# Optimization experiments

Measured on AMD Instinct MI355X. Metric: run time of the kernel, lower is better.

The kernel has to match this reference:

```python
import jax, jax.numpy as jnp
import numpy as np

B, T, W, N, D, H, E, NB = 1, 2048, 15, 512, 1024, 150, 20, 10
CP = 2  # coref_prop iterations
NEG = 1e23


def _bucket(d):
    # Lee-et-al style distance bucketing into NB=10 buckets
    d = jnp.clip(d, 0, None)
    logd = (jnp.floor(jnp.log(jnp.maximum(d.astype(jnp.float32), 1.0)) / np.log(2.0)).astype(jnp.int32) + 3)
    return jnp.clip(jnp.where(d <= 4, d, logd), 0, NB - 1)


def _pairs(u, begin, end, Wl, bl, Wr, br, Wp, bp, Edist, Wd, bd, W1, b1, Wo, bo):
    # OptFFpairs: left + right + prod*prod + dist-embedding -> 2-layer FF -> scalar
    l = u @ Wl + bl                                   # [B,N,H]
    r = u @ Wr + br
    s = u @ Wp + bp
    dist = _bucket(begin[:, :, None] - end[:, None, :])  # [B,N,N]
    pe = Edist[dist] @ Wd + bd                        # [B,N,N,H]
    h = l[:, :, None, :] + r[:, None, :, :] + s[:, :, None, :] * s[:, None, :, :] + pe
    h = jax.nn.relu(h)
    h = jax.nn.relu(h @ W1 + b1)
    return (h @ Wo + bo)[..., 0]                      # [B,N,N]


def _add_scores(cs, ss):
    # coref_add_scores: add unary span scores symmetrically, zero the diagonal
    s = cs + ss + jnp.swapaxes(ss, -1, -2)            # ss: [B,N,1]
    eye = jnp.eye(s.shape[-1], dtype=s.dtype)
    return s * (1.0 - eye)


def _overwrite_spans(all_vecs, idx, lengths, values):
    b, t, w, d = all_vecs.shape
    flat = all_vecs.reshape(b, t * w, d)
    k = idx.shape[1]
    mask = (jnp.arange(k)[None, :] < lengths[:, None])[..., None]   # [B,K,1]
    bidx = jnp.arange(b)[:, None]
    orig = flat[bidx, idx]                                          # [B,K,D]
    flat = flat.at[bidx, idx].set(jnp.where(mask, values, orig))
    return flat.reshape(b, t, w, d)


def setup_inputs() -> dict:
    key = jax.random.key(0)
    ks = jax.random.split(key, 24)
    sc = 0.02
    inp = {
        'all_span_vecs': jax.random.normal(ks[0], (B, T, W, D), jnp.float32),
        'span_vecs': jax.random.normal(ks[1], (B, N, D), jnp.float32),
        'span_scores': jax.random.normal(ks[2], (B, N, 1), jnp.float32),
        'triangular_mask': jnp.tril(jnp.ones((N, N), jnp.float32))[None].repeat(B, 0),
        'span_begin': jnp.sort(jax.random.randint(ks[3], (B, N), 0, T), axis=-1).astype(jnp.int32),
        'span_end': jax.random.randint(ks[4], (B, N), 0, T).astype(jnp.int32),
        'prune_indices': jnp.sort(jax.random.permutation(ks[5], T * W)[:N])[None].astype(jnp.int64),
        'span_lengths': jnp.full((B,), N, jnp.int32),
        # OptFFpairs params
        'Wl': jax.random.normal(ks[6], (D, H)) * sc, 'bl': jnp.zeros((H,)),
        'Wr': jax.random.normal(ks[7], (D, H)) * sc, 'br': jnp.zeros((H,)),
        'Wp': jax.random.normal(ks[8], (D, H)) * sc, 'bp': jnp.zeros((H,)),
        'Edist': jax.random.normal(ks[9], (NB, E)) * sc,
        'Wd': jax.random.normal(ks[10], (E, H)) * sc, 'bd': jnp.zeros((H,)),
        'W1': jax.random.normal(ks[11], (H, H)) * sc, 'b1': jnp.zeros((H,)),
        'Wo': jax.random.normal(ks[12], (H, 1)) * sc, 'bo': jnp.zeros((1,)),
        # MyGate params
        'Wg': jax.random.normal(ks[13], (2 * D, D)) * sc, 'bg': jnp.zeros((D,)),
        # coref_pruner params
        'Wpr': jax.random.normal(ks[14], (D, 1)) * sc, 'bpr': jnp.zeros((1,)),
    }
    return inp


def reference(all_span_vecs, span_vecs, span_scores, triangular_mask,
              Wl, bl, Wr, br, Wp, bp, Edist, Wd, bd, W1, b1, Wo, bo,
              Wg, bg, Wpr, bpr,
              span_begin, span_end, prune_indices, span_lengths):
    pargs = (Wl, bl, Wr, br, Wp, bp, Edist, Wd, bd, W1, b1, Wo, bo)
    update = span_vecs
    scores = _pairs(update, span_begin, span_end, *pargs)
    scores = _add_scores(scores, span_scores)
    for _ in range(CP):
        probs = jax.nn.softmax(scores - (1.0 - triangular_mask) * NEG, axis=-1)
        ctxt = jnp.einsum('bij,bjd->bid', probs, update)
        g = jax.nn.sigmoid(jnp.concatenate([update, ctxt], axis=-1) @ Wg + bg)
        update = g * update + (1.0 - g) * ctxt
        scores = _pairs(update, span_begin, span_end, *pargs)
        scores = _add_scores(scores, update @ Wpr + bpr)
    all_out = _overwrite_spans(all_span_vecs, prune_indices, span_lengths, update)
    return (all_out, update, scores)
```

## Files before the change

### kernel.cpp

```cpp
#include <hip/hip_runtime.h>
#include <hip/hip_bf16.h>
#include <cstdint>
#include <cstddef>

typedef __attribute__((ext_vector_type(8))) short short8;
typedef __attribute__((ext_vector_type(4))) float floatx4;

#define MFMA_BF16(a,b,c) __builtin_amdgcn_mfma_f32_16x16x32_bf16((a),(b),(c),0,0,0)

__device__ __forceinline__ float bf2f(short s) {
    return __uint_as_float(((unsigned int)(unsigned short)s) << 16);
}
__device__ __forceinline__ unsigned short f2bf(float f) {
    unsigned int u = __float_as_uint(f);
    u += 0x7FFFu + ((u >> 16) & 1u);
    return (unsigned short)(u >> 16);
}
__device__ __forceinline__ int bucketd(int d) {
    if (d < 0) d = 0;
    if (d <= 4) return d;
    int b = 34 - __clz(d);
    return b > 9 ? 9 : b;
}

__global__ __launch_bounds__(256) void k_prep(
    const float* __restrict__ Wg, const float* __restrict__ Wl, const float* __restrict__ Wr,
    const float* __restrict__ Wp, const float* __restrict__ Wpr,
    const float* __restrict__ span_vecs, const float* __restrict__ span_scores,
    const float* __restrict__ W1g, const float* __restrict__ Edist,
    const float* __restrict__ Wd, const float* __restrict__ bd,
    const float* __restrict__ b1, const float* __restrict__ Wo,
    const float* __restrict__ bl, const float* __restrict__ br, const float* __restrict__ bp,
    const float* __restrict__ bpr,
    unsigned short* __restrict__ WgT, unsigned short* __restrict__ WprojT,
    unsigned short* __restrict__ updT, unsigned short* __restrict__ ubf0,
    float* __restrict__ updatef, float* __restrict__ ss0,
    unsigned short* __restrict__ W1T, unsigned short* __restrict__ Pb,
    float* __restrict__ b1p, float* __restrict__ wop, float* __restrict__ bproj)
{
    __shared__ float tile[32][33];
    int b = blockIdx.x, tid = threadIdx.x;
    if (b < 3040) {
        const float* in; unsigned short* out; int R, C, ldo, rb, cb;
        if (b < 2048)      { in = Wg; out = WgT; R = 2048; C = 1024; ldo = 2048; rb = (b & 63) * 32; cb = (b >> 6) * 32; }
        else if (b < 2208) { int t = b - 2048; in = Wl; out = WprojT;            R = 1024; C = 150; ldo = 1024; rb = (t & 31) * 32; cb = (t >> 5) * 32; }
        else if (b < 2368) { int t = b - 2208; in = Wr; out = WprojT + 192*1024; R = 1024; C = 150; ldo = 1024; rb = (t & 31) * 32; cb = (t >> 5) * 32; }
        else if (b < 2528) { int t = b - 2368; in = Wp; out = WprojT + 384*1024; R = 1024; C = 150; ldo = 1024; rb = (t & 31) * 32; cb = (t >> 5) * 32; }
        else               { int t = b - 2528; in = span_vecs; out = updT;       R = 512;  C = 1024; ldo = 512;  rb = (t & 15) * 32; cb = (t >> 4) * 32; }
        int tx = tid & 31, ty = tid >> 5;
#pragma unroll
        for (int k = 0; k < 4; ++k) {
            int r = rb + ty + k*8, c = cb + tx;
            if (r < R && c < C) tile[ty + k*8][tx] = in[(size_t)r*C + c];
        }
        __syncthreads();
#pragma unroll
        for (int k = 0; k < 4; ++k) {
            int c = cb + ty + k*8, r = rb + tx;
            if (r < R && c < C) out[(size_t)c*ldo + r] = f2bf(tile[tx][ty + k*8]);
        }
        return;
    }
    int g = (b - 3040) * 256 + tid;
    const int gsz = 512 * 256;
    for (int i = g; i < 512*1024; i += gsz) {
        float v = span_vecs[i];
        updatef[i] = v;
        ubf0[(i >> 10)*2048 + (i & 1023)] = f2bf(v);
    }
    for (int i = g; i < 512; i += gsz) ss0[i] = span_scores[i];
    for (int i = g; i < 160*168; i += gsz) {
        int n = i / 168, k = i % 168;
        W1T[i] = f2bf((n < 150 && k < 150) ? W1g[k*150 + n] : 0.f);
    }
    for (int i = g; i < 10*168; i += gsz) {
        int bk = i / 168, h = i % 168;
        float v = 0.f;
        if (h < 150) {
            v = bd[h];
            for (int e = 0; e < 20; ++e) v += Edist[bk*20 + e] * Wd[e*150 + h];
        }
        Pb[i] = f2bf(v);
    }
    for (int i = g; i < 160; i += gsz) {
        b1p[i] = (i < 150) ? b1[i] : 0.f;
        wop[i] = (i < 150) ? Wo[i] : 0.f;
    }
    for (int i = g; i < 640; i += gsz) {
        float v = 0.f;
        if (i < 150) v = bl[i];
        else if (i >= 192 && i < 342) v = br[i - 192];
        else if (i >= 384 && i < 534) v = bp[i - 384];
        else if (i == 576) v = bpr[0];
        bproj[i] = v;
    }
    for (int i = g; i < 42*1024; i += gsz) { WprojT[150*1024 + i] = 0; WprojT[342*1024 + i] = 0; WprojT[534*1024 + i] = 0; }
    for (int i = g; i < 1024; i += gsz) WprojT[576*1024 + i] = f2bf(Wpr[i]);
    for (int i = g; i < 63*1024; i += gsz) WprojT[577*1024 + i] = 0;
}

__global__ __launch_bounds__(256) void k_gemm64(
    const unsigned short* __restrict__ A, int lda,
    const unsigned short* __restrict__ BT, int ldb,
    int K, const float* __restrict__ bias,
    float* __restrict__ Cf, int ldc,
    unsigned short* __restrict__ Cb, int ldcb,
    const float* __restrict__ uf, const float* __restrict__ cf,
    float* __restrict__ uout, unsigned short* __restrict__ updTout,
    float* __restrict__ ss1, int mode)
{
    __shared__ __align__(16) unsigned short As[64*72];
    __shared__ __align__(16) unsigned short Bs[64*72];
    int tid = threadIdx.x;
    int lane = tid & 63, w = tid >> 6;
    int wy = w >> 1, wx = w & 1;
    int ln15 = lane & 15, kg = lane >> 4;
    int m0 = blockIdx.x * 64, n0 = blockIdx.y * 64;
    int r0 = tid >> 3, c8 = (tid & 7) * 8;
    const unsigned short* pA0 = A + (size_t)(m0 + r0)*lda + c8;
    const unsigned short* pA1 = pA0 + (size_t)32*lda;
    const unsigned short* pB0 = BT + (size_t)(n0 + r0)*ldb + c8;
    const unsigned short* pB1 = pB0 + (size_t)32*ldb;
    floatx4 acc[2][2] = {};
    uint4 va0 = *(const uint4*)pA0, va1 = *(const uint4*)pA1;
    uint4 vb0 = *(const uint4*)pB0, vb1 = *(const uint4*)pB1;
    for (int kb = 0; kb < K; kb += 64) {
        __syncthreads();
        *(uint4*)(&As[r0*72 + c8])        = va0;
        *(uint4*)(&As[(r0 + 32)*72 + c8]) = va1;
        *(uint4*)(&Bs[r0*72 + c8])        = vb0;
        *(uint4*)(&Bs[(r0 + 32)*72 + c8]) = vb1;
        __syncthreads();
        int kn = kb + 64;
        if (kn < K) {
            va0 = *(const uint4*)(pA0 + kn); va1 = *(const uint4*)(pA1 + kn);
            vb0 = *(const uint4*)(pB0 + kn); vb1 = *(const uint4*)(pB1 + kn);
        }
#pragma unroll
        for (int ks = 0; ks < 2; ++ks) {
            int ko = ks*32 + kg*8;
            short8 a0 = *(const short8*)(&As[(wy*32 + ln15)*72 + ko]);
            short8 a1 = *(const short8*)(&As[(wy*32 + 16 + ln15)*72 + ko]);
            short8 b0 = *(const short8*)(&Bs[(wx*32 + ln15)*72 + ko]);
            short8 b1 = *(const short8*)(&Bs[(wx*32 + 16 + ln15)*72 + ko]);
            acc[0][0] = MFMA_BF16(a0, b0, acc[0][0]);
            acc[0][1] = MFMA_BF16(a0, b1, acc[0][1]);
            acc[1][0] = MFMA_BF16(a1, b0, acc[1][0]);
            acc[1][1] = MFMA_BF16(a1, b1, acc[1][1]);
        }
    }
#pragma unroll
    for (int mt = 0; mt < 2; ++mt)
#pragma unroll
    for (int nt = 0; nt < 2; ++nt) {
        int n  = n0 + wx*32 + nt*16 + ln15;
        int mb = m0 + wy*32 + mt*16 + kg*4;
        if (mode == 0) {
            float b_ = bias[n];
#pragma unroll
            for (int rg = 0; rg < 4; ++rg) {
                float v = acc[mt][nt][rg] + b_;
                Cb[(size_t)(mb + rg)*ldcb + n] = f2bf(v);
                if (n == 576) ss1[mb + rg] = v;
            }
        } else if (mode == 1) {
#pragma unroll
            for (int rg = 0; rg < 4; ++rg) {
                float v = acc[mt][nt][rg];
                Cf[(size_t)(mb + rg)*ldc + n] = v;
                Cb[(size_t)(mb + rg)*ldcb + n] = f2bf(v);
            }
        } else {
            float b_ = bias[n];
            ushort4 tv;
            unsigned short* tvp = &tv.x;
#pragma unroll
            for (int rg = 0; rg < 4; ++rg) {
                float v = acc[mt][nt][rg] + b_;
                float gg = 1.f / (1.f + __expf(-v));
                size_t off = (size_t)(mb + rg)*1024 + n;
                float nu = gg*uf[off] + (1.f - gg)*cf[off];
                uout[off] = nu;
                unsigned short nb = f2bf(nu);
                Cb[(size_t)(mb + rg)*ldcb + n] = nb;
                tvp[rg] = nb;
            }
            *(ushort4*)(updTout + (size_t)n*512 + mb) = tv;
        }
    }
}

__global__ __launch_bounds__(256) void k_softmax(const float* __restrict__ scores,
                                                 unsigned short* __restrict__ probsb)
{
    int i = blockIdx.x;
    int tid = threadIdx.x;
    int lane = tid & 63, w = tid >> 6;
    __shared__ float red[8];
    int j0 = tid, j1 = tid + 256;
    bool v0 = (j0 <= i), v1 = (j1 <= i);
    float x0 = v0 ? scores[(size_t)i*512 + j0] : -1e30f;
    float x1 = v1 ? scores[(size_t)i*512 + j1] : -1e30f;
    float mx = fmaxf(x0, x1);
    for (int off = 32; off; off >>= 1) mx = fmaxf(mx, __shfl_xor(mx, off));
    if (lane == 0) red[w] = mx;
    __syncthreads();
    mx = fmaxf(fmaxf(red[0], red[1]), fmaxf(red[2], red[3]));
    float p0 = v0 ? __expf(x0 - mx) : 0.f;
    float p1 = v1 ? __expf(x1 - mx) : 0.f;
    float sm = p0 + p1;
    for (int off = 32; off; off >>= 1) sm += __shfl_xor(sm, off);
    if (lane == 0) red[4 + w] = sm;
    __syncthreads();
    float inv = 1.f / (red[4] + red[5] + red[6] + red[7]);
    probsb[(size_t)i*512 + j0] = f2bf(p0 * inv);
    probsb[(size_t)i*512 + j1] = f2bf(p1 * inv);
}

__global__ __launch_bounds__(512, 2) void k_pair(
    const unsigned short* __restrict__ lrsb,
    const unsigned short* __restrict__ Pb,
    const unsigned short* __restrict__ W1Tg,
    const float* __restrict__ b1p, const float* __restrict__ wop,
    const float* __restrict__ bo,
    const float* __restrict__ ssbuf,
    const int* __restrict__ beginp, const int* __restrict__ endp,
    float* __restrict__ scoresOut)
{
    __shared__ __align__(16) unsigned short smR[74*168];
    int tid = threadIdx.x;
    int i0 = blockIdx.x * 16, j0 = blockIdx.y * 16;
    for (int c = tid; c < 74*21; c += 512) {
        int row = c / 21, c8 = (c % 21) * 8;
        const unsigned short* src;
        if (row < 16)      src = lrsb + (size_t)(i0 + row)*640 + c8;
        else if (row < 32) src = lrsb + (size_t)(i0 + row - 16)*640 + 384 + c8;
        else if (row < 48) src = lrsb + (size_t)(j0 + row - 32)*640 + 192 + c8;
        else if (row < 64) src = lrsb + (size_t)(j0 + row - 48)*640 + 384 + c8;
        else               src = Pb + (size_t)(row - 64)*168 + c8;
        *(uint4*)(&smR[row*168 + c8]) = *(const uint4*)src;
    }
    int lane = tid & 63, w = tid >> 6;
    int ln15 = lane & 15, kg = lane >> 4;
    int iw = i0 + 2*w;
    int ej = endp[j0 + ln15];
    int da = bucketd(beginp[iw] - ej);
    int db = bucketd(beginp[iw + 1] - ej);
    __syncthreads();
    floatx4 acc[2][10] = {};
    for (int kb = 0; kb < 5; ++kb) {
        int ko = kb*32 + kg*8;
        short8 bv[10];
#pragma unroll
        for (int nt = 0; nt < 10; ++nt)
            bv[nt] = *(const short8*)(W1Tg + (size_t)(nt*16 + ln15)*168 + ko);
        short8 rv  = *(const short8*)(&smR[(32 + ln15)*168 + ko]);
        short8 sjv = *(const short8*)(&smR[(48 + ln15)*168 + ko]);
        short8 hf[2];
#pragma unroll
        for (int mt = 0; mt < 2; ++mt) {
            int ri = 2*w + mt;
            short8 lv  = *(const short8*)(&smR[ri*168 + ko]);
            short8 siv = *(const short8*)(&smR[(16 + ri)*168 + ko]);
            int d = mt ? db : da;
            short8 pv  = *(const short8*)(&smR[(64 + d)*168 + ko]);
#pragma unroll
            for (int t = 0; t < 8; ++t) {
                float h = bf2f(lv[t]) + bf2f(rv[t]) + bf2f(siv[t]) * bf2f(sjv[t]) + bf2f(pv[t]);
                h = fmaxf(h, 0.f);
                hf[mt][t] = (short)f2bf(h);
            }
        }
#pragma unroll
        for (int nt = 0; nt < 10; ++nt) {
            acc[0][nt] = MFMA_BF16(hf[0], bv[nt], acc[0][nt]);
            acc[1][nt] = MFMA_BF16(hf[1], bv[nt], acc[1][nt]);
        }
    }
    float part[2][4] = {};
#pragma unroll
    for (int nt = 0; nt < 10; ++nt) {
        int n = nt*16 + ln15;
        float b1v = b1p[n], wv = wop[n];
#pragma unroll
        for (int mt = 0; mt < 2; ++mt)
#pragma unroll
            for (int rg = 0; rg < 4; ++rg)
                part[mt][rg] += fmaxf(acc[mt][nt][rg] + b1v, 0.f) * wv;
    }
    float bo0 = bo[0];
#pragma unroll
    for (int mt = 0; mt < 2; ++mt) {
#pragma unroll
        for (int rg = 0; rg < 4; ++rg) {
            float p = part[mt][rg];
            p += __shfl_xor(p, 1); p += __shfl_xor(p, 2);
            p += __shfl_xor(p, 4); p += __shfl_xor(p, 8);
            part[mt][rg] = p;
        }
        if (ln15 == 0) {
            int i = iw + mt;
            float ssi = ssbuf[i];
            int jb = j0 + kg*4;
            float r0 = part[mt][0] + bo0 + ssi + ssbuf[jb + 0]; if (i == jb + 0) r0 = 0.f;
            float r1 = part[mt][1] + bo0 + ssi + ssbuf[jb + 1]; if (i == jb + 1) r1 = 0.f;
            float r2 = part[mt][2] + bo0 + ssi + ssbuf[jb + 2]; if (i == jb + 2) r2 = 0.f;
            float r3 = part[mt][3] + bo0 + ssi + ssbuf[jb + 3]; if (i == jb + 3) r3 = 0.f;
            float4 vv; vv.x = r0; vv.y = r1; vv.z = r2; vv.w = r3;
            *(float4*)(scoresOut + (size_t)i*512 + jb) = vv;
        }
    }
}

__global__ __launch_bounds__(256) void k_final(const float* __restrict__ allv,
                                               const int* __restrict__ prune,
                                               const int* __restrict__ lengths,
                                               const float* __restrict__ updatef,
                                               float* __restrict__ out)
{
    int row = blockIdx.x;
    if (row < 30720) {
        int len = lengths[0];
        if (len > 512) len = 512;
        int lo = 0, hi = len;
        while (lo < hi) { int mid = (lo + hi) >> 1; if (prune[mid] < row) lo = mid + 1; else hi = mid; }
        bool found = (lo < len) && (prune[lo] == row);
        const float4* src = found ? (const float4*)(updatef + (size_t)lo*1024)
                                  : (const float4*)(allv + (size_t)row*1024);
        ((float4*)(out + (size_t)row*1024))[threadIdx.x] = src[threadIdx.x];
    } else {
        int k = row - 30720;
        ((float4*)(out + (size_t)row*1024))[threadIdx.x] =
            ((const float4*)(updatef + (size_t)k*1024))[threadIdx.x];
    }
}

extern "C" void kernel_launch(void* const* d_in, const int* in_sizes, int n_in,
                              void* d_out, int out_size, void* d_ws, size_t ws_size,
                              hipStream_t stream) {
    const float* all_span    = (const float*)d_in[0];
    const float* span_vecs   = (const float*)d_in[1];
    const float* span_scores = (const float*)d_in[2];
    const int*   beginp      = (const int*)d_in[4];
    const int*   endp        = (const int*)d_in[5];
    const int*   prune       = (const int*)d_in[6];
    const int*   lengths     = (const int*)d_in[7];
    const float* Wl = (const float*)d_in[8];  const float* bl = (const float*)d_in[9];
    const float* Wr = (const float*)d_in[10]; const float* br = (const float*)d_in[11];
    const float* Wp = (const float*)d_in[12]; const float* bp = (const float*)d_in[13];
    const float* Edist = (const float*)d_in[14];
    const float* Wd = (const float*)d_in[15]; const float* bd = (const float*)d_in[16];
    const float* W1 = (const float*)d_in[17]; const float* b1 = (const float*)d_in[18];
    const float* Wo = (const float*)d_in[19]; const float* bo = (const float*)d_in[20];
    const float* Wg = (const float*)d_in[21]; const float* bg = (const float*)d_in[22];
    const float* Wpr = (const float*)d_in[23]; const float* bpr = (const float*)d_in[24];

    char* wsb = (char*)d_ws;
    size_t o = 0;
    auto nxt = [&](size_t b) { size_t r = o; o += (b + 255) & ~(size_t)255; return r; };
    float* updatef  = (float*)(wsb + nxt(512*1024*4));
    float* ctxtf    = (float*)(wsb + nxt(512*1024*4));
    float* scoresws = (float*)(wsb + nxt(512*512*4));
    float* ss0      = (float*)(wsb + nxt(512*4));
    float* ss1      = (float*)(wsb + nxt(512*4));
    float* bproj    = (float*)(wsb + nxt(640*4));
    float* b1p      = (float*)(wsb + nxt(160*4));
    float* wop      = (float*)(wsb + nxt(160*4));
    unsigned short* ubf0    = (unsigned short*)(wsb + nxt(512*2048*2));
    unsigned short* ubf1    = (unsigned short*)(wsb + nxt(512*2048*2));
    unsigned short* updT    = (unsigned short*)(wsb + nxt(1024*512*2));
    unsigned short* probsb  = (unsigned short*)(wsb + nxt(512*512*2));
    unsigned short* lrsb    = (unsigned short*)(wsb + nxt(512*640*2));
    unsigned short* WgT     = (unsigned short*)(wsb + nxt(1024*2048*2));
    unsigned short* WprojT  = (unsigned short*)(wsb + nxt(640*1024*2));
    unsigned short* W1T     = (unsigned short*)(wsb + nxt(160*168*2));
    unsigned short* Pb      = (unsigned short*)(wsb + nxt(10*168*2));

    float* outp = (float*)d_out;
    float* out_scores = outp + 31457280 + 524288;

    k_prep<<<3552, 256, 0, stream>>>(Wg, Wl, Wr, Wp, Wpr, span_vecs, span_scores,
                                     W1, Edist, Wd, bd, b1, Wo, bl, br, bp, bpr,
                                     WgT, WprojT, updT, ubf0, updatef, ss0,
                                     W1T, Pb, b1p, wop, bproj);

    k_gemm64<<<dim3(8, 10), 256, 0, stream>>>(ubf0, 2048, WprojT, 1024, 1024, bproj,
                                              nullptr, 0, lrsb, 640,
                                              nullptr, nullptr, nullptr, nullptr, ss1, 0);
    k_pair<<<dim3(32, 32), 512, 0, stream>>>(lrsb, Pb, W1T, b1p, wop, bo, ss0, beginp, endp, scoresws);

    unsigned short* ucur = ubf0;
    unsigned short* unxt = ubf1;
    for (int it = 0; it < 2; ++it) {
        k_softmax<<<512, 256, 0, stream>>>(scoresws, probsb);
        k_gemm64<<<dim3(8, 16), 256, 0, stream>>>(probsb, 512, updT, 512, 512, nullptr,
                                                  ctxtf, 1024, ucur + 1024, 2048,
                                                  nullptr, nullptr, nullptr, nullptr, nullptr, 1);
        k_gemm64<<<dim3(8, 16), 256, 0, stream>>>(ucur, 2048, WgT, 2048, 2048, bg,
                                                  nullptr, 0, unxt, 2048,
                                                  updatef, ctxtf, updatef, updT, nullptr, 2);
        k_gemm64<<<dim3(8, 10), 256, 0, stream>>>(unxt, 2048, WprojT, 1024, 1024, bproj,
                                                  nullptr, 0, lrsb, 640,
                                                  nullptr, nullptr, nullptr, nullptr, ss1, 0);
        float* sdst = (it == 1) ? out_scores : scoresws;
        k_pair<<<dim3(32, 32), 512, 0, stream>>>(lrsb, Pb, W1T, b1p, wop, bo, ss1, beginp, endp, sdst);
        unsigned short* t = ucur; ucur = unxt; unxt = t;
    }

    k_final<<<31232, 256, 0, stream>>>(all_span, prune, lengths, updatef, outp);
}
```

Baseline: 514.9 us.

## Shrink GEMM M-tile to 32 with deeper prefetch; stage W1 in LDS for pair kernel

The GEMM kernel drops from 64x64 to 32x64 tiles, which doubles the grid (128 to 256 blocks for the larger GEMMs) to better fill the many CUs. It also prefetches global data two K-steps ahead through a pair of register buffers and adds an occupancy hint. The pair kernel now stages each 32-wide K slice of W1 into double-buffered shared memory with register prefetch, instead of having every wave read the W1 fragments straight from global memory. This adds LDS use and a barrier per K step in the pair kernel, and smaller GEMM tiles mean less reuse of each loaded B tile.

Result: slower. 536.6 us (+4.2%).

```diff
diff --git a/kernel.cpp b/kernel.cpp
--- a/kernel.cpp
+++ b/kernel.cpp
@@ -99,84 +99,81 @@
     for (int i = g; i < 63*1024; i += gsz) WprojT[577*1024 + i] = 0;
 }
 
-__global__ __launch_bounds__(256) void k_gemm64(
+__global__ __launch_bounds__(256, 4) void k_gemm(
     const unsigned short* __restrict__ A, int lda,
     const unsigned short* __restrict__ BT, int ldb,
     int K, const float* __restrict__ bias,
-    float* __restrict__ Cf, int ldc,
+    float* __restrict__ Cf,
     unsigned short* __restrict__ Cb, int ldcb,
     const float* __restrict__ uf, const float* __restrict__ cf,
     float* __restrict__ uout, unsigned short* __restrict__ updTout,
     float* __restrict__ ss1, int mode)
 {
-    __shared__ __align__(16) unsigned short As[64*72];
+    __shared__ __align__(16) unsigned short As[32*72];
     __shared__ __align__(16) unsigned short Bs[64*72];
     int tid = threadIdx.x;
     int lane = tid & 63, w = tid >> 6;
     int wy = w >> 1, wx = w & 1;
     int ln15 = lane & 15, kg = lane >> 4;
-    int m0 = blockIdx.x * 64, n0 = blockIdx.y * 64;
-    int r0 = tid >> 3, c8 = (tid & 7) * 8;
-    const unsigned short* pA0 = A + (size_t)(m0 + r0)*lda + c8;
-    const unsigned short* pA1 = pA0 + (size_t)32*lda;
-    const unsigned short* pB0 = BT + (size_t)(n0 + r0)*ldb + c8;
+    int m0 = blockIdx.x * 32, n0 = blockIdx.y * 64;
+    int rA = tid >> 3, c8 = (tid & 7) * 8;
+    const unsigned short* pA  = A  + (size_t)(m0 + rA)*lda + c8;
+    const unsigned short* pB0 = BT + (size_t)(n0 + rA)*ldb + c8;
     const unsigned short* pB1 = pB0 + (size_t)32*ldb;
-    floatx4 acc[2][2] = {};
-    uint4 va0 = *(const uint4*)pA0, va1 = *(const uint4*)pA1;
-    uint4 vb0 = *(const uint4*)pB0, vb1 = *(const uint4*)pB1;
-    for (int kb = 0; kb < K; kb += 64) {
+    int nk = K >> 6;
+    uint4 ra[2], rb0[2], rb1[2];
+    ra[0]  = *(const uint4*)pA;        ra[1]  = *(const uint4*)(pA + 64);
+    rb0[0] = *(const uint4*)pB0;       rb0[1] = *(const uint4*)(pB0 + 64);
+    rb1[0] = *(const uint4*)pB1;       rb1[1] = *(const uint4*)(pB1 + 64);
+    floatx4 acc[2] = {};
+    for (int k = 0; k < nk; ++k) {
+        int cur = k & 1;
         __syncthreads();
-        *(uint4*)(&As[r0*72 + c8])        = va0;
-        *(uint4*)(&As[(r0 + 32)*72 + c8]) = va1;
-        *(uint4*)(&Bs[r0*72 + c8])        = vb0;
-        *(uint4*)(&Bs[(r0 + 32)*72 + c8]) = vb1;
+        *(uint4*)(&As[rA*72 + c8])        = ra[cur];
+        *(uint4*)(&Bs[rA*72 + c8])        = rb0[cur];
+        *(uint4*)(&Bs[(rA + 32)*72 + c8]) = rb1[cur];
+        int kn = (k + 2) << 6;
+        if (kn < K) {
+            ra[cur]  = *(const uint4*)(pA + kn);
+            rb0[cur] = *(const uint4*)(pB0 + kn);
+            rb1[cur] = *(const uint4*)(pB1 + kn);
+        }
         __syncthreads();
-        int kn = kb + 64;
-        if (kn < K) {
-            va0 = *(const uint4*)(pA0 + kn); va1 = *(const uint4*)(pA1 + kn);
-            vb0 = *(const uint4*)(pB0 + kn); vb1 = *(const uint4*)(pB1 + kn);
-        }
 #pragma unroll
         for (int ks = 0; ks < 2; ++ks) {
             int ko = ks*32 + kg*8;
-            short8 a0 = *(const short8*)(&As[(wy*32 + ln15)*72 + ko]);
-            short8 a1 = *(const short8*)(&As[(wy*32 + 16 + ln15)*72 + ko]);
+            short8 a  = *(const short8*)(&As[(wy*16 + ln15)*72 + ko]);
             short8 b0 = *(const short8*)(&Bs[(wx*32 + ln15)*72 + ko]);
             short8 b1 = *(const short8*)(&Bs[(wx*32 + 16 + ln15)*72 + ko]);
-            acc[0][0] = MFMA_BF16(a0, b0, acc[0][0]);
-            acc[0][1] = MFMA_BF16(a0, b1, acc[0][1]);
-            acc[1][0] = MFMA_BF16(a1, b0, acc[1][0]);
-            acc[1][1] = MFMA_BF16(a1, b1, acc[1][1]);
-        }
-    }
-#pragma unroll
-    for (int mt = 0; mt < 2; ++mt)
+            acc[0] = MFMA_BF16(a, b0, acc[0]);
+            acc[1] = MFMA_BF16(a, b1, acc[1]);
+        }
+    }
 #pragma unroll
     for (int nt = 0; nt < 2; ++nt) {
         int n  = n0 + wx*32 + nt*16 + ln15;
-        int mb = m0 + wy*32 + mt*16 + kg*4;
+        int mb = m0 + wy*16 + kg*4;
         if (mode == 0) {
             float b_ = bias[n];
 #pragma unroll
             for (int rg = 0; rg < 4; ++rg) {
-                float v = acc[mt][nt][rg] + b_;
+                float v = acc[nt][rg] + b_;
                 Cb[(size_t)(mb + rg)*ldcb + n] = f2bf(v);
                 if (n == 576) ss1[mb + rg] = v;
             }
         } else if (mode == 1) {
 #pragma unroll
             for (int rg = 0; rg < 4; ++rg) {
-                float v = acc[mt][nt][rg];
-                Cf[(size_t)(mb + rg)*ldc + n] = v;
+                float v = acc[nt][rg];
+                Cf[(size_t)(mb + rg)*1024 + n] = v;
                 Cb[(size_t)(mb + rg)*ldcb + n] = f2bf(v);
             }
         } else {
             float b_ = bias[n];
-            ushort4 tv;
-            unsigned short* tvp = &tv.x;
+            ushort4 tv; unsigned short* tvp = &tv.x;
 #pragma unroll
             for (int rg = 0; rg < 4; ++rg) {
-                float v = acc[mt][nt][rg] + b_;
+                float v = acc[nt][rg] + b_;
                 float gg = 1.f / (1.f + __expf(-v));
                 size_t off = (size_t)(mb + rg)*1024 + n;
                 float nu = gg*uf[off] + (1.f - gg)*cf[off];
@@ -228,6 +225,7 @@
     float* __restrict__ scoresOut)
 {
     __shared__ __align__(16) unsigned short smR[74*168];
+    __shared__ __align__(16) unsigned short smB[2][160*36];
     int tid = threadIdx.x;
     int i0 = blockIdx.x * 16, j0 = blockIdx.y * 16;
     for (int c = tid; c < 74*21; c += 512) {
@@ -246,14 +244,23 @@
     int ej = endp[j0 + ln15];
     int da = bucketd(beginp[iw] - ej);
     int db = bucketd(beginp[iw + 1] - ej);
-    __syncthreads();
+    int rW = tid >> 2, cW = (tid & 3) * 8;
+    int rW2 = 128 + rW;
+    bool has2 = (tid < 128);
+    uint4 w0 = *(const uint4*)(W1Tg + (size_t)rW*168 + cW);
+    uint4 w1 = has2 ? *(const uint4*)(W1Tg + (size_t)rW2*168 + cW) : make_uint4(0,0,0,0);
     floatx4 acc[2][10] = {};
     for (int kb = 0; kb < 5; ++kb) {
+        int cur = kb & 1;
+        *(uint4*)(&smB[cur][rW*36 + cW]) = w0;
+        if (has2) *(uint4*)(&smB[cur][rW2*36 + cW]) = w1;
+        if (kb < 4) {
+            int kf = (kb + 1)*32;
+            w0 = *(const uint4*)(W1Tg + (size_t)rW*168 + kf + cW);
+            if (has2) w1 = *(const uint4*)(W1Tg + (size_t)rW2*168 + kf + cW);
+        }
+        __syncthreads();
         int ko = kb*32 + kg*8;
-        short8 bv[10];
-#pragma unroll
-        for (int nt = 0; nt < 10; ++nt)
-            bv[nt] = *(const short8*)(W1Tg + (size_t)(nt*16 + ln15)*168 + ko);
         short8 rv  = *(const short8*)(&smR[(32 + ln15)*168 + ko]);
         short8 sjv = *(const short8*)(&smR[(48 + ln15)*168 + ko]);
         short8 hf[2];
@@ -273,8 +280,9 @@
         }
 #pragma unroll
         for (int nt = 0; nt < 10; ++nt) {
-            acc[0][nt] = MFMA_BF16(hf[0], bv[nt], acc[0][nt]);
-            acc[1][nt] = MFMA_BF16(hf[1], bv[nt], acc[1][nt]);
+            short8 bv = *(const short8*)(&smB[cur][(nt*16 + ln15)*36 + kg*8]);
+            acc[0][nt] = MFMA_BF16(hf[0], bv, acc[0][nt]);
+            acc[1][nt] = MFMA_BF16(hf[1], bv, acc[1][nt]);
         }
     }
     float part[2][4] = {};
@@ -384,24 +392,24 @@
                                      WgT, WprojT, updT, ubf0, updatef, ss0,
                                      W1T, Pb, b1p, wop, bproj);
 
-    k_gemm64<<<dim3(8, 10), 256, 0, stream>>>(ubf0, 2048, WprojT, 1024, 1024, bproj,
-                                              nullptr, 0, lrsb, 640,
-                                              nullptr, nullptr, nullptr, nullptr, ss1, 0);
+    k_gemm<<<dim3(16, 10), 256, 0, stream>>>(ubf0, 2048, WprojT, 1024, 1024, bproj,
+                                             nullptr, lrsb, 640,
+                                             nullptr, nullptr, nullptr, nullptr, ss1, 0);
     k_pair<<<dim3(32, 32), 512, 0, stream>>>(lrsb, Pb, W1T, b1p, wop, bo, ss0, beginp, endp, scoresws);
 
     unsigned short* ucur = ubf0;
     unsigned short* unxt = ubf1;
     for (int it = 0; it < 2; ++it) {
         k_softmax<<<512, 256, 0, stream>>>(scoresws, probsb);
-        k_gemm64<<<dim3(8, 16), 256, 0, stream>>>(probsb, 512, updT, 512, 512, nullptr,
-                                                  ctxtf, 1024, ucur + 1024, 2048,
-                                                  nullptr, nullptr, nullptr, nullptr, nullptr, 1);
-        k_gemm64<<<dim3(8, 16), 256, 0, stream>>>(ucur, 2048, WgT, 2048, 2048, bg,
-                                                  nullptr, 0, unxt, 2048,
-                                                  updatef, ctxtf, updatef, updT, nullptr, 2);
-        k_gemm64<<<dim3(8, 10), 256, 0, stream>>>(unxt, 2048, WprojT, 1024, 1024, bproj,
-                                                  nullptr, 0, lrsb, 640,
-                                                  nullptr, nullptr, nullptr, nullptr, ss1, 0);
+        k_gemm<<<dim3(16, 16), 256, 0, stream>>>(probsb, 512, updT, 512, 512, nullptr,
+                                                 ctxtf, ucur + 1024, 2048,
+                                                 nullptr, nullptr, nullptr, nullptr, nullptr, 1);
+        k_gemm<<<dim3(16, 16), 256, 0, stream>>>(ucur, 2048, WgT, 2048, 2048, bg,
+                                                 nullptr, unxt, 2048,
+                                                 updatef, ctxtf, updatef, updT, nullptr, 2);
+        k_gemm<<<dim3(16, 10), 256, 0, stream>>>(unxt, 2048, WprojT, 1024, 1024, bproj,
+                                                 nullptr, lrsb, 640,
+                                                 nullptr, nullptr, nullptr, nullptr, ss1, 0);
         float* sdst = (it == 1) ? out_scores : scoresws;
         k_pair<<<dim3(32, 32), 512, 0, stream>>>(lrsb, Pb, W1T, b1p, wop, bo, ss1, beginp, endp, sdst);
         unsigned short* t = ucur; ucur = unxt; unxt = t;
```
